# Optimization experiments

Hardware: AMD Instinct MI355X
Metric: run time of the kernel (lower is better)

## Reference

```python
import jax, jax.numpy as jnp
import numpy as np

N_NODES = 10242
BN_EPS = 1e-5


def _conv(x, idx, w, W, b):
    # x: [N, C]; idx: [N*25*3] int; w: [N, 25, 3]; W: [Cout, 25*C]; b: [Cout]
    n = x.shape[0]
    mat = x[idx].reshape(n, 25, 3, -1)                 # gather: [N,25,3,C]
    agg = jnp.einsum('nkte,nkt->nke', mat, w)          # weighted interp sum over 3 verts
    agg = agg.reshape(n, -1)                           # [N, 25*C]
    return agg @ W.T + b


def _bn_relu(x, g, be):
    # BatchNorm1d in training mode: batch (node-axis) stats, biased variance
    mu = jnp.mean(x, axis=0)
    var = jnp.var(x, axis=0)
    return jax.nn.relu((x - mu) * jax.lax.rsqrt(var + BN_EPS) * g + be)


def setup_inputs() -> dict:
    key = jax.random.key(0)
    ks = jax.random.split(key, 16)
    inp = {}
    inp['x'] = jax.random.normal(ks[0], (N_NODES, 3), dtype=jnp.float32)
    inp['neigh_indices'] = jax.random.randint(ks[1], (N_NODES * 25 * 3,), 0, N_NODES, dtype=jnp.int32)
    w = jax.random.uniform(ks[2], (N_NODES, 25, 3), dtype=jnp.float32)
    inp['neigh_weights'] = w / jnp.sum(w, axis=-1, keepdims=True)  # barycentric-like weights
    def lin(k, cout, cin):
        s = 1.0 / np.sqrt(cin)
        return (jax.random.uniform(k, (cout, cin), dtype=jnp.float32, minval=-s, maxval=s),)
    inp['W1'], = lin(ks[3], 64, 25 * 3);   inp['b1'] = jnp.zeros((64,), jnp.float32)
    inp['g1'] = jnp.ones((64,), jnp.float32);  inp['be1'] = jnp.zeros((64,), jnp.float32)
    inp['W2'], = lin(ks[4], 64, 25 * 64);  inp['b2'] = jnp.zeros((64,), jnp.float32)
    inp['g2'] = jnp.ones((64,), jnp.float32);  inp['be2'] = jnp.zeros((64,), jnp.float32)
    inp['W3'], = lin(ks[5], 128, 25 * 64); inp['b3'] = jnp.zeros((128,), jnp.float32)
    inp['g3'] = jnp.ones((128,), jnp.float32); inp['be3'] = jnp.zeros((128,), jnp.float32)
    inp['Wout'], = lin(ks[6], 36, 25 * 128); inp['bout'] = jnp.zeros((36,), jnp.float32)
    return inp


def reference(x, neigh_indices, neigh_weights, W1, b1, g1, be1, W2, b2, g2, be2,
              W3, b3, g3, be3, Wout, bout):
    h = _bn_relu(_conv(x, neigh_indices, neigh_weights, W1, b1), g1, be1)
    h = _bn_relu(_conv(h, neigh_indices, neigh_weights, W2, b2), g2, be2)
    h = _bn_relu(_conv(h, neigh_indices, neigh_weights, W3, b3), g3, be3)
    out = _conv(h, neigh_indices, neigh_weights, Wout, bout)   # [N, num_classes]
    return out
```

## Files before the change

### kernel.cpp

```cpp
#include <hip/hip_runtime.h>

#define NN 10242

typedef short s8v __attribute__((ext_vector_type(8)));
typedef unsigned int u32x4 __attribute__((ext_vector_type(4)));
typedef float f32x4 __attribute__((ext_vector_type(4)));

static __device__ __forceinline__ float bf2f(unsigned short u) {
    unsigned int i = ((unsigned int)u) << 16;
    return __builtin_bit_cast(float, i);
}
static __device__ __forceinline__ unsigned short f2bf(float f) {
    unsigned int i = __builtin_bit_cast(unsigned int, f);
    unsigned int lsb = (i >> 16) & 1u;
    i += 0x7fffu + lsb;
    return (unsigned short)(i >> 16);
}
static __device__ __forceinline__ unsigned int cvtpk(float lo, float hi) {
    unsigned int r;
    asm("v_cvt_pk_bf16_f32 %0, %1, %2" : "=v"(r) : "v"(lo), "v"(hi));
    return r;
}
static __device__ __forceinline__ void gl_lds16(const unsigned short* g, unsigned short* l) {
    __builtin_amdgcn_global_load_lds(
        (const __attribute__((address_space(1))) unsigned int*)g,
        (__attribute__((address_space(3))) unsigned int*)l, 16, 0, 0);
}
template<int N> static __device__ __forceinline__ void waitv() {
    asm volatile("s_waitcnt vmcnt(%0)" :: "n"(N) : "memory");
    __builtin_amdgcn_sched_barrier(0);
}
static __device__ __forceinline__ int imin(int a, int b) { return a < b ? a : b; }

__global__ void detect_k(const void* __restrict__ wgt, int* __restrict__ flag) {
    const float* wf = (const float*)wgt;
    const int r = threadIdx.x;
    float s = wf[3 * r] + wf[3 * r + 1] + wf[3 * r + 2];
    bool ok = (s == s) && (fabsf(s - 1.f) < 0.05f);
    unsigned long long m = __ballot(ok);
    if (r == 0) *flag = (__popcll(m) >= 60) ? 1 : 0;
}

struct Seg { const void* src; void* dst; int n; int nsrc; int mode; int K; int cout; int cpad; };
struct Tab { Seg s[16]; };

__global__ __launch_bounds__(256) void canon_k(Tab t, const int* __restrict__ flag) {
    const Seg sg = t.s[blockIdx.y];
    const bool f32src = (*flag != 0);
    for (int i = blockIdx.x * 256 + threadIdx.x; i < sg.n; i += gridDim.x * 256) {
        if (sg.mode == 0) {
            unsigned short v = 0;
            if (i < sg.nsrc)
                v = f32src ? f2bf(((const float*)sg.src)[i])
                           : ((const unsigned short*)sg.src)[i];
            ((unsigned short*)sg.dst)[i] = v;
        } else if (sg.mode == 1) {
            float v = f32src ? ((const float*)sg.src)[i]
                             : bf2f(((const unsigned short*)sg.src)[i]);
            ((float*)sg.dst)[i] = v;
        } else if (sg.mode == 2) {
            const int row = i / 80, col = i - row * 80;
            unsigned short v = 0;
            if (col < 75) {
                const int j = row * 75 + col;
                v = f32src ? f2bf(((const float*)sg.src)[j])
                           : ((const unsigned short*)sg.src)[j];
            }
            ((unsigned short*)sg.dst)[i] = v;
        } else {
            const int e = i & 7;
            const int r = i >> 3;
            const int c = r % sg.cpad;
            const int k8 = r / sg.cpad;
            unsigned short v = 0;
            if (c < sg.cout) {
                const int j = c * sg.K + k8 * 8 + e;
                v = f32src ? f2bf(((const float*)sg.src)[j])
                           : ((const unsigned short*)sg.src)[j];
            }
            ((unsigned short*)sg.dst)[i] = v;
        }
    }
}

template<int CIN, int COUT, int CG, int NB>
__global__ __launch_bounds__(256) void conv_k(
    const unsigned short* __restrict__ X,
    const int* __restrict__ idx,
    const float* __restrict__ wgt,
    const unsigned short* __restrict__ W,
    const float* __restrict__ bias,
    float* __restrict__ Of)
{
    constexpr int K = 25 * CIN;
    constexpr int KPAD = (K + 7) & ~7;
    __shared__ unsigned short agg[NB][KPAD];
    const int tid = threadIdx.x;
    const int n0 = blockIdx.x * NB;

    for (int p = tid; p < NB * 25; p += 256) {
        const int r = p / 25;
        const int k = p - r * 25;
        const int n = n0 + r;
        if (n < NN) {
            const int base = n * 75 + k * 3;
            const int i0 = idx[base], i1 = idx[base + 1], i2 = idx[base + 2];
            const float w0 = wgt[base], w1 = wgt[base + 1], w2 = wgt[base + 2];
            for (int e = 0; e < CIN; e++) {
                float v = w0 * bf2f(X[i0 * CIN + e]) +
                          w1 * bf2f(X[i1 * CIN + e]) +
                          w2 * bf2f(X[i2 * CIN + e]);
                agg[r][k * CIN + e] = f2bf(v);
            }
        } else {
            for (int e = 0; e < CIN; e++) agg[r][k * CIN + e] = 0;
        }
    }
    if constexpr (KPAD != K) {
        for (int p = tid; p < NB * (KPAD - K); p += 256) {
            const int r = p / (KPAD - K);
            agg[r][K + p - r * (KPAD - K)] = 0;
        }
    }
    __syncthreads();

    constexpr int RG = 256 / CG;
    constexpr int RPT = NB / RG;
    const int c = tid % CG;
    const int rq = tid / CG;
    float acc[RPT] = {};
    if (c < COUT) {
        const unsigned short* Wr = W + (size_t)c * KPAD;
        for (int j = 0; j < KPAD; j += 8) {
            s8v wv = *(const s8v*)(Wr + j);
            float wf[8];
            #pragma unroll
            for (int q = 0; q < 8; q++) wf[q] = bf2f((unsigned short)wv[q]);
            #pragma unroll
            for (int rr = 0; rr < RPT; rr++) {
                s8v av = *(const s8v*)(&agg[rq * RPT + rr][j]);
                #pragma unroll
                for (int q = 0; q < 8; q++)
                    acc[rr] += wf[q] * bf2f((unsigned short)av[q]);
            }
        }
        const float bb = bias[c];
        #pragma unroll
        for (int rr = 0; rr < RPT; rr++) {
            const int n = n0 + rq * RPT + rr;
            if (n < NN) Of[(size_t)n * COUT + c] = acc[rr] + bb;
        }
    }
}

template<int CIN, int COUTP, int COUT, bool FINAL>
__global__ __launch_bounds__(256, 2) void convdma_k(
    const unsigned short* __restrict__ X,
    const int* __restrict__ idx,
    const float* __restrict__ wgt,
    const unsigned short* __restrict__ Wt,
    const float* __restrict__ bias,
    float* __restrict__ pre,
    void* __restrict__ Ob,
    const int* __restrict__ flag)
{
    constexpr int NT = CIN / 32;
    constexpr int NFRAG = COUTP / 64;
    constexpr int INSTS = CIN / 8;
    constexpr int Q = INSTS / 4;
    constexpr int R = NT * NFRAG;
    __shared__ unsigned short raw[4 * 64 * CIN];
    __shared__ int   iL[25 * 64];
    __shared__ float wL[25 * 48];
    const int tid = threadIdx.x;
    const int n0 = blockIdx.x * 16;

    for (int q = tid; q < 16 * 75; q += 256) {
        const int node = q / 75, f = q - node * 75;
        const int k = f / 3, v = f - k * 3;
        const int n = n0 + node;
        const bool ok = n < NN;
        const int g = ok ? (n * 75 + f) : 0;
        iL[k * 64 + node * 4 + v] = ok ? idx[g] : 0;
        wL[k * 48 + node * 3 + v] = ok ? wgt[g] : 0.f;
    }
    for (int q = tid; q < 25 * 16; q += 256)
        iL[(q / 16) * 64 + (q - (q / 16) * 16) * 4 + 3] = 0;
    __syncthreads();

    const int wv = tid >> 6;
    const int lane = tid & 63;
    const int l15 = lane & 15;
    const int kg = lane >> 4;
    const int colbase = wv * NFRAG * 16;

    auto issue = [&](int sd) {
        const int base = (sd & 3) * (64 * CIN);
        #pragma unroll
        for (int jj = 0; jj < Q; jj++) {
            const int j = wv * Q + jj;
            int row, p;
            if constexpr (CIN == 64) { row = j * 8 + (lane >> 3); p = lane & 7; }
            else                     { row = j * 4 + (lane >> 4); p = lane & 15; }
            const int ch = p ^ ((row >> 2) & 7);
            const int id = iL[sd * 64 + row];
            gl_lds16(X + (size_t)id * CIN + ch * 8, &raw[base + j * 512]);
        }
    };
    auto loadB = [&](int sp, s8v* dst) {
        #pragma unroll
        for (int t = 0; t < NT; t++)
            #pragma unroll
            for (int j = 0; j < NFRAG; j++)
                dst[t * NFRAG + j] = *(const s8v*)(Wt +
                    ((size_t)(sp * (CIN / 8) + t * 4 + kg) * COUTP + colbase + j * 16 + l15) * 8);
    };

    f32x4 acc[NFRAG] = {};
    s8v breg[2][R];

    issue(0);
    loadB(0, breg[0]);
    issue(1);
    issue(2);

    #pragma unroll
    for (int s = 0; s < 25; s++) {
        __builtin_amdgcn_s_barrier();
        if (s + 1 < 25) loadB(s + 1, breg[(s + 1) & 1]);
        if (s + 3 < 25) issue(s + 3);
        if (s == 0)       waitv<3 * Q + R>();
        else if (s < 22)  waitv<2 * Q + R>();
        else if (s == 22) waitv<Q + R>();
        else if (s == 23) waitv<R>();
        else              waitv<0>();
        __builtin_amdgcn_s_barrier();
        const int rb = (s & 3) * (64 * CIN) + l15 * 4 * CIN;
        const float w0 = wL[s * 48 + l15 * 3 + 0];
        const float w1 = wL[s * 48 + l15 * 3 + 1];
        const float w2 = wL[s * 48 + l15 * 3 + 2];
        #pragma unroll
        for (int t = 0; t < NT; t++) {
            const int p = (t * 4 + kg) ^ (l15 & 7);
            const s8v va = *(const s8v*)(&raw[rb + 0 * CIN + p * 8]);
            const s8v vb = *(const s8v*)(&raw[rb + 1 * CIN + p * 8]);
            const s8v vc = *(const s8v*)(&raw[rb + 2 * CIN + p * 8]);
            u32x4 au;
            #pragma unroll
            for (int qq = 0; qq < 4; qq++) {
                const float lo = w0 * bf2f((unsigned short)va[2 * qq]) +
                                 w1 * bf2f((unsigned short)vb[2 * qq]) +
                                 w2 * bf2f((unsigned short)vc[2 * qq]);
                const float hi = w0 * bf2f((unsigned short)va[2 * qq + 1]) +
                                 w1 * bf2f((unsigned short)vb[2 * qq + 1]) +
                                 w2 * bf2f((unsigned short)vc[2 * qq + 1]);
                au[qq] = cvtpk(lo, hi);
            }
            const s8v a = __builtin_bit_cast(s8v, au);
            #pragma unroll
            for (int j = 0; j < NFRAG; j++)
                acc[j] = __builtin_amdgcn_mfma_f32_16x16x32_bf16(a, breg[s & 1][t * NFRAG + j], acc[j], 0, 0, 0);
        }
    }

    bool f32o = false;
    if constexpr (FINAL) f32o = (*flag != 0);
    #pragma unroll
    for (int j = 0; j < NFRAG; j++) {
        const int col = colbase + j * 16 + l15;
        if (col < COUT) {
            const float bb = bias[col];
            #pragma unroll
            for (int q = 0; q < 4; q++) {
                const int n = n0 + kg * 4 + q;
                if (n < NN) {
                    const float v = acc[j][q] + bb;
                    if constexpr (FINAL) {
                        if (f32o) ((float*)Ob)[(size_t)n * COUT + col] = v;
                        else ((unsigned short*)Ob)[(size_t)n * COUT + col] = f2bf(v);
                    } else {
                        pre[(size_t)n * COUT + col] = v;
                    }
                }
            }
        }
    }
}

template<int C>
__global__ __launch_bounds__(256) void stats_k(const float* __restrict__ pre,
                                               float* __restrict__ part)
{
    constexpr int RG = 256 / C;
    constexpr int CH = (NN + 63) / 64;
    const int b = blockIdx.x;
    const int r0 = b * CH;
    const int r1 = imin(NN, r0 + CH);
    const int c = threadIdx.x % C;
    const int g = threadIdx.x / C;
    float s = 0.f, s2 = 0.f;
    for (int r = r0 + g; r < r1; r += RG) {
        float v = pre[(size_t)r * C + c];
        s += v; s2 += v * v;
    }
    __shared__ float ls[256], ls2[256];
    ls[threadIdx.x] = s; ls2[threadIdx.x] = s2;
    __syncthreads();
    if (threadIdx.x < C) {
        float a = 0.f, a2 = 0.f;
        #pragma unroll
        for (int g2 = 0; g2 < RG; g2++) {
            a  += ls[g2 * C + threadIdx.x];
            a2 += ls2[g2 * C + threadIdx.x];
        }
        part[b * 2 * C + threadIdx.x] = a;
        part[b * 2 * C + C + threadIdx.x] = a2;
    }
}

template<int C>
__global__ __launch_bounds__(256) void bn_k(const float* __restrict__ pre,
                                            const float* __restrict__ part,
                                            const float* __restrict__ gm,
                                            const float* __restrict__ bt,
                                            unsigned short* __restrict__ act)
{
    __shared__ float sc[C], sh[C];
    if (threadIdx.x < C) {
        const int c = threadIdx.x;
        float s = 0.f, s2 = 0.f;
        for (int b = 0; b < 64; b++) {
            s  += part[b * 2 * C + c];
            s2 += part[b * 2 * C + C + c];
        }
        const float inv = 1.f / (float)NN;
        float mu = s * inv;
        float var = s2 * inv - mu * mu;
        float scale = gm[c] * rsqrtf(var + 1e-5f);
        sc[c] = scale;
        sh[c] = bt[c] - mu * scale;
    }
    __syncthreads();
    const int chunk = (NN + gridDim.x - 1) / gridDim.x;
    const int r0 = blockIdx.x * chunk;
    const int r1 = imin(NN, r0 + chunk);
    for (int i = r0 * C + threadIdx.x; i < r1 * C; i += 256) {
        const int c = i % C;
        float v = fmaxf(pre[i] * sc[c] + sh[c], 0.f);
        act[i] = f2bf(v);
    }
}

extern "C" void kernel_launch(void* const* d_in, const int* in_sizes, int n_in,
                              void* d_out, int out_size, void* d_ws, size_t ws_size,
                              hipStream_t stream) {
    const void* x    = d_in[0];
    const int*  idx  = (const int*)d_in[1];
    const void* wgt  = d_in[2];
    const void* W1   = d_in[3];
    const void* b1   = d_in[4];
    const void* g1   = d_in[5];
    const void* be1  = d_in[6];
    const void* W2   = d_in[7];
    const void* b2   = d_in[8];
    const void* g2   = d_in[9];
    const void* be2  = d_in[10];
    const void* W3   = d_in[11];
    const void* b3   = d_in[12];
    const void* g3   = d_in[13];
    const void* be3  = d_in[14];
    const void* Wout = d_in[15];
    const void* bout = d_in[16];

    char* ws = (char*)d_ws;
    size_t off = 0;
    auto alloc = [&](size_t bytes) {
        off = (off + 255) & ~(size_t)255;
        size_t o = off; off += bytes; return o;
    };
    const size_t o_flag = alloc(4);
    const size_t o_xc   = alloc((size_t)NN * 3 * 2);
    const size_t o_wgtc = alloc((size_t)NN * 75 * 4);
    const size_t o_W1c  = alloc(64 * 80 * 2);
    const size_t o_Wt2  = alloc((size_t)200 * 64 * 8 * 2);
    const size_t o_Wt3  = alloc((size_t)200 * 128 * 8 * 2);
    const size_t o_Wt4  = alloc((size_t)400 * 64 * 8 * 2);
    const size_t o_bias = alloc(1024 * 4);
    const size_t o_pre  = alloc((size_t)NN * 128 * 4);
    const size_t o_actA = alloc((size_t)NN * 128 * 2);
    const size_t o_actB = alloc((size_t)NN * 64 * 2);
    const size_t o_part = alloc((size_t)64 * 2 * 128 * 4);
    if (ws_size < off) return;

    int* flag = (int*)(ws + o_flag);
    unsigned short* xc  = (unsigned short*)(ws + o_xc);
    float* wgtc = (float*)(ws + o_wgtc);
    unsigned short* W1c = (unsigned short*)(ws + o_W1c);
    unsigned short* Wt2 = (unsigned short*)(ws + o_Wt2);
    unsigned short* Wt3 = (unsigned short*)(ws + o_Wt3);
    unsigned short* Wt4 = (unsigned short*)(ws + o_Wt4);
    float* biasc = (float*)(ws + o_bias);
    float* pre  = (float*)(ws + o_pre);
    unsigned short* actA = (unsigned short*)(ws + o_actA);
    unsigned short* actB = (unsigned short*)(ws + o_actB);
    float* part = (float*)(ws + o_part);

    detect_k<<<1, 64, 0, stream>>>(wgt, flag);

    Tab t;
    t.s[0]  = { x,    xc,   NN * 3,         NN * 3,  0, 0, 0, 0 };
    t.s[1]  = { wgt,  wgtc, NN * 75,        NN * 75, 1, 0, 0, 0 };
    t.s[2]  = { W1,   W1c,  64 * 80,        64 * 80, 2, 0, 0, 0 };
    t.s[3]  = { W2,   Wt2,  200 * 64 * 8,   0,       3, 1600, 64, 64 };
    t.s[4]  = { W3,   Wt3,  200 * 128 * 8,  0,       3, 1600, 128, 128 };
    t.s[5]  = { Wout, Wt4,  400 * 64 * 8,   0,       3, 3200, 36, 64 };
    t.s[6]  = { b1,   biasc + 0,   64, 64, 1, 0, 0, 0 };
    t.s[7]  = { g1,   biasc + 64,  64, 64, 1, 0, 0, 0 };
    t.s[8]  = { be1,  biasc + 128, 64, 64, 1, 0, 0, 0 };
    t.s[9]  = { b2,   biasc + 192, 64, 64, 1, 0, 0, 0 };
    t.s[10] = { g2,   biasc + 256, 64, 64, 1, 0, 0, 0 };
    t.s[11] = { be2,  biasc + 320, 64, 64, 1, 0, 0, 0 };
    t.s[12] = { b3,   biasc + 384, 128, 128, 1, 0, 0, 0 };
    t.s[13] = { g3,   biasc + 512, 128, 128, 1, 0, 0, 0 };
    t.s[14] = { be3,  biasc + 640, 128, 128, 1, 0, 0, 0 };
    t.s[15] = { bout, biasc + 768, 36, 36, 1, 0, 0, 0 };
    canon_k<<<dim3(768, 16), 256, 0, stream>>>(t, flag);

    dim3 B(256);
    conv_k<3, 64, 64, 16><<<641, B, 0, stream>>>(xc, idx, wgtc, W1c, biasc + 0, pre);
    stats_k<64><<<64, B, 0, stream>>>(pre, part);
    bn_k<64><<<128, B, 0, stream>>>(pre, part, biasc + 64, biasc + 128, actA);
    convdma_k<64, 64, 64, false><<<641, B, 0, stream>>>(
        actA, idx, wgtc, Wt2, biasc + 192, pre, nullptr, flag);
    stats_k<64><<<64, B, 0, stream>>>(pre, part);
    bn_k<64><<<128, B, 0, stream>>>(pre, part, biasc + 256, biasc + 320, actB);
    convdma_k<64, 128, 128, false><<<641, B, 0, stream>>>(
        actB, idx, wgtc, Wt3, biasc + 384, pre, nullptr, flag);
    stats_k<128><<<64, B, 0, stream>>>(pre, part);
    bn_k<128><<<128, B, 0, stream>>>(pre, part, biasc + 512, biasc + 640, actA);
    convdma_k<128, 64, 36, true><<<641, B, 0, stream>>>(
        actA, idx, wgtc, Wt4, biasc + 768, nullptr, d_out, flag);
}
```

Before: 194.7 us.

## Split gather interpolation into cooperative LDS pass and add configurable ring depth

The 3-vertex weighted interpolation moves out of the per-wave MFMA operand path into a cooperative pass. All 256 threads each interpolate a few elements once into a double-buffered bf16 agg tile in LDS. The waves then read MFMA A-fragments directly from that tile. Before, every wave redundantly recomputed the interpolation for the same 16 nodes. The change also drops the XOR swizzle, adds a RING template (2 stages for the CIN=128 final layer, 4 otherwise), reorders loads and waits, and raises launch bounds to 3 blocks/SM. The extra barrier, the LDS round trip and the unswizzled layout may add bank conflicts or sync cost.

```diff
diff --git a/kernel.cpp b/kernel.cpp
--- a/kernel.cpp
+++ b/kernel.cpp
@@ -3,12 +3,18 @@
 #define NN 10242
 
 typedef short s8v __attribute__((ext_vector_type(8)));
-typedef unsigned int u32x4 __attribute__((ext_vector_type(4)));
+typedef unsigned int u32x2 __attribute__((ext_vector_type(2)));
 typedef float f32x4 __attribute__((ext_vector_type(4)));
 
 static __device__ __forceinline__ float bf2f(unsigned short u) {
     unsigned int i = ((unsigned int)u) << 16;
     return __builtin_bit_cast(float, i);
+}
+static __device__ __forceinline__ float bfu32lo(unsigned int d) {
+    return __builtin_bit_cast(float, d << 16);
+}
+static __device__ __forceinline__ float bfu32hi(unsigned int d) {
+    return __builtin_bit_cast(float, d & 0xffff0000u);
 }
 static __device__ __forceinline__ unsigned short f2bf(float f) {
     unsigned int i = __builtin_bit_cast(unsigned int, f);
@@ -28,6 +34,10 @@
 }
 template<int N> static __device__ __forceinline__ void waitv() {
     asm volatile("s_waitcnt vmcnt(%0)" :: "n"(N) : "memory");
+    __builtin_amdgcn_sched_barrier(0);
+}
+static __device__ __forceinline__ void lgkm0() {
+    asm volatile("s_waitcnt lgkmcnt(0)" ::: "memory");
     __builtin_amdgcn_sched_barrier(0);
 }
 static __device__ __forceinline__ int imin(int a, int b) { return a < b ? a : b; }
@@ -153,8 +163,8 @@
     }
 }
 
-template<int CIN, int COUTP, int COUT, bool FINAL>
-__global__ __launch_bounds__(256, 2) void convdma_k(
+template<int CIN, int COUTP, int COUT, int RING, bool FINAL>
+__global__ __launch_bounds__(256, 3) void convdma2_k(
     const unsigned short* __restrict__ X,
     const int* __restrict__ idx,
     const float* __restrict__ wgt,
@@ -169,7 +179,10 @@
     constexpr int INSTS = CIN / 8;
     constexpr int Q = INSTS / 4;
     constexpr int R = NT * NFRAG;
-    __shared__ unsigned short raw[4 * 64 * CIN];
+    constexpr int UPNS = (CIN == 64) ? 4 : 5;
+    constexpr int UNITS = 16 << UPNS;
+    __shared__ unsigned short raw[RING * 64 * CIN];
+    __shared__ unsigned short agg[2][16][CIN + 8];
     __shared__ int   iL[25 * 64];
     __shared__ float wL[25 * 48];
     const int tid = threadIdx.x;
@@ -195,16 +208,15 @@
     const int colbase = wv * NFRAG * 16;
 
     auto issue = [&](int sd) {
-        const int base = (sd & 3) * (64 * CIN);
+        const int base = (sd & (RING - 1)) * (64 * CIN);
         #pragma unroll
         for (int jj = 0; jj < Q; jj++) {
             const int j = wv * Q + jj;
             int row, p;
             if constexpr (CIN == 64) { row = j * 8 + (lane >> 3); p = lane & 7; }
             else                     { row = j * 4 + (lane >> 4); p = lane & 15; }
-            const int ch = p ^ ((row >> 2) & 7);
             const int id = iL[sd * 64 + row];
-            gl_lds16(X + (size_t)id * CIN + ch * 8, &raw[base + j * 512]);
+            gl_lds16(X + (size_t)id * CIN + p * 8, &raw[base + j * 512]);
         }
     };
     auto loadB = [&](int sp, s8v* dst) {
@@ -219,47 +231,58 @@
     f32x4 acc[NFRAG] = {};
     s8v breg[2][R];
 
-    issue(0);
-    loadB(0, breg[0]);
-    issue(1);
-    issue(2);
+    if constexpr (RING == 4) { issue(0); issue(1); loadB(0, breg[0]); issue(2); }
+    else                     { issue(0); loadB(0, breg[0]); issue(1); }
 
     #pragma unroll
     for (int s = 0; s < 25; s++) {
+        if (s + 1 < 25) loadB(s + 1, breg[(s + 1) & 1]);
+        if constexpr (RING == 4) {
+            if (s <= 22)      waitv<2 * Q + 2 * R>();
+            else if (s == 23) waitv<Q + 2 * R>();
+            else              waitv<R>();
+        } else {
+            if (s <= 23)      waitv<Q + 2 * R>();
+            else              waitv<R>();
+        }
         __builtin_amdgcn_s_barrier();
-        if (s + 1 < 25) loadB(s + 1, breg[(s + 1) & 1]);
-        if (s + 3 < 25) issue(s + 3);
-        if (s == 0)       waitv<3 * Q + R>();
-        else if (s < 22)  waitv<2 * Q + R>();
-        else if (s == 22) waitv<Q + R>();
-        else if (s == 23) waitv<R>();
-        else              waitv<0>();
+        {
+            const int sb = (s & (RING - 1)) * (64 * CIN);
+            #pragma unroll
+            for (int u = tid; u < UNITS; u += 256) {
+                const int node = u >> UPNS;
+                const int e4 = u & ((1 << UPNS) - 1);
+                const float w0 = wL[s * 48 + node * 3 + 0];
+                const float w1 = wL[s * 48 + node * 3 + 1];
+                const float w2 = wL[s * 48 + node * 3 + 2];
+                const int rb = sb + node * 4 * CIN + e4 * 4;
+                const u32x2 A = *(const u32x2*)&raw[rb + 0 * CIN];
+                const u32x2 B = *(const u32x2*)&raw[rb + 1 * CIN];
+                const u32x2 C = *(const u32x2*)&raw[rb + 2 * CIN];
+                const float v0 = w0 * bfu32lo(A[0]) + w1 * bfu32lo(B[0]) + w2 * bfu32lo(C[0]);
+                const float v1 = w0 * bfu32hi(A[0]) + w1 * bfu32hi(B[0]) + w2 * bfu32hi(C[0]);
+                const float v2 = w0 * bfu32lo(A[1]) + w1 * bfu32lo(B[1]) + w2 * bfu32lo(C[1]);
+                const float v3 = w0 * bfu32hi(A[1]) + w1 * bfu32hi(B[1]) + w2 * bfu32hi(C[1]);
+                u32x2 o;
+                o[0] = cvtpk(v0, v1);
+                o[1] = cvtpk(v2, v3);
+                *(u32x2*)&agg[s & 1][node][e4 * 4] = o;
+            }
+        }
+        if constexpr (RING == 4) { if (s + 3 < 25) issue(s + 3); }
+        lgkm0();
         __builtin_amdgcn_s_barrier();
-        const int rb = (s & 3) * (64 * CIN) + l15 * 4 * CIN;
-        const float w0 = wL[s * 48 + l15 * 3 + 0];
-        const float w1 = wL[s * 48 + l15 * 3 + 1];
-        const float w2 = wL[s * 48 + l15 * 3 + 2];
+        if constexpr (RING == 2) {
+            if (s + 2 < 25) issue(s + 2);
+            __builtin_amdgcn_sched_barrier(0);
+        }
         #pragma unroll
         for (int t = 0; t < NT; t++) {
-            const int p = (t * 4 + kg) ^ (l15 & 7);
-            const s8v va = *(const s8v*)(&raw[rb + 0 * CIN + p * 8]);
-            const s8v vb = *(const s8v*)(&raw[rb + 1 * CIN + p * 8]);
-            const s8v vc = *(const s8v*)(&raw[rb + 2 * CIN + p * 8]);
-            u32x4 au;
-            #pragma unroll
-            for (int qq = 0; qq < 4; qq++) {
-                const float lo = w0 * bf2f((unsigned short)va[2 * qq]) +
-                                 w1 * bf2f((unsigned short)vb[2 * qq]) +
-                                 w2 * bf2f((unsigned short)vc[2 * qq]);
-                const float hi = w0 * bf2f((unsigned short)va[2 * qq + 1]) +
-                                 w1 * bf2f((unsigned short)vb[2 * qq + 1]) +
-                                 w2 * bf2f((unsigned short)vc[2 * qq + 1]);
-                au[qq] = cvtpk(lo, hi);
-            }
-            const s8v a = __builtin_bit_cast(s8v, au);
+            const s8v a = *(const s8v*)(&agg[s & 1][l15][t * 32 + kg * 8]);
             #pragma unroll
             for (int j = 0; j < NFRAG; j++)
-                acc[j] = __builtin_amdgcn_mfma_f32_16x16x32_bf16(a, breg[s & 1][t * NFRAG + j], acc[j], 0, 0, 0);
+                acc[j] = __builtin_amdgcn_mfma_f32_16x16x32_bf16(
+                    a, breg[s & 1][t * NFRAG + j], acc[j], 0, 0, 0);
         }
     }
 
@@ -430,14 +453,14 @@
     conv_k<3, 64, 64, 16><<<641, B, 0, stream>>>(xc, idx, wgtc, W1c, biasc + 0, pre);
     stats_k<64><<<64, B, 0, stream>>>(pre, part);
     bn_k<64><<<128, B, 0, stream>>>(pre, part, biasc + 64, biasc + 128, actA);
-    convdma_k<64, 64, 64, false><<<641, B, 0, stream>>>(
+    convdma2_k<64, 64, 64, 4, false><<<641, B, 0, stream>>>(
         actA, idx, wgtc, Wt2, biasc + 192, pre, nullptr, flag);
     stats_k<64><<<64, B, 0, stream>>>(pre, part);
     bn_k<64><<<128, B, 0, stream>>>(pre, part, biasc + 256, biasc + 320, actB);
-    convdma_k<64, 128, 128, false><<<641, B, 0, stream>>>(
+    convdma2_k<64, 128, 128, 4, false><<<641, B, 0, stream>>>(
         actB, idx, wgtc, Wt3, biasc + 384, pre, nullptr, flag);
     stats_k<128><<<64, B, 0, stream>>>(pre, part);
     bn_k<128><<<128, B, 0, stream>>>(pre, part, biasc + 512, biasc + 640, actA);
-    convdma_k<128, 64, 36, true><<<641, B, 0, stream>>>(
+    convdma2_k<128, 64, 36, 2, true><<<641, B, 0, stream>>>(
         actA, idx, wgtc, Wt4, biasc + 768, nullptr, d_out, flag);
 }
```

Result: faster. 162.5 us (-16.5%).
